# Kernel tuning notes

Hardware: AMD Instinct MI355X
Metric: run time of the kernel (lower is better)

The kernel has to match this reference:

```python
import jax, jax.numpy as jnp
import numpy as np

B, T = 256, 512
D_L, D_T, D_W, D_S = 64, 32, 32, 32
XPRIME, HIDDEN = 256, 512


def setup_inputs() -> dict:
    key = jax.random.key(0)
    ks = jax.random.split(key, 11)
    s = 0.05
    return {
        "x_l_seq": jax.random.normal(ks[0], (B, T, D_L), jnp.float32),
        "x_t_seq": jax.random.normal(ks[1], (B, T, D_T), jnp.float32),
        "x_w_seq": jax.random.normal(ks[2], (B, T, D_W), jnp.float32),
        "x_s_seq": jax.random.normal(ks[3], (B, T, D_S), jnp.float32),
        "W_ih": jax.random.normal(ks[4], (3 * HIDDEN, XPRIME), jnp.float32) * s,
        "W_hh": jax.random.normal(ks[5], (3 * HIDDEN, HIDDEN), jnp.float32) * s,
        "b_ih": jax.random.normal(ks[6], (3 * HIDDEN,), jnp.float32) * s,
        "b_hh": jax.random.normal(ks[7], (3 * HIDDEN,), jnp.float32) * s,
        "Wt_h": jax.random.normal(ks[8], (XPRIME, HIDDEN), jnp.float32) * s,
        "Wt_x": jax.random.normal(ks[9], (XPRIME, D_L + D_T + D_W + D_S), jnp.float32) * s,
        "bt": jax.random.normal(ks[10], (XPRIME,), jnp.float32) * s,
    }


def reference(x_l_seq, x_t_seq, x_w_seq, x_s_seq, W_ih, W_hh, b_ih, b_hh, Wt_h, Wt_x, bt):
    # concat the four feature streams once: [B, T, D_tot]
    x_cat = jnp.concatenate([x_l_seq, x_t_seq, x_w_seq, x_s_seq], axis=-1)
    H = W_hh.shape[1]
    Bb = x_cat.shape[0]

    def step(h, x_t):  # h: [B,H], x_t: [B,D_tot]
        # transform_block: per-step meta transform fused with recurrence
        x_prime = jnp.tanh(h @ Wt_h.T + x_t @ Wt_x.T + bt)  # [B, XPRIME]
        # torch nn.GRU cell (gate order r, z, n)
        gx = x_prime @ W_ih.T + b_ih  # [B, 3H]
        gh = h @ W_hh.T + b_hh        # [B, 3H]
        xr, xz, xn = gx[:, :H], gx[:, H:2 * H], gx[:, 2 * H:]
        hr, hz, hn = gh[:, :H], gh[:, H:2 * H], gh[:, 2 * H:]
        r = jax.nn.sigmoid(xr + hr)
        z = jax.nn.sigmoid(xz + hz)
        n = jnp.tanh(xn + r * hn)
        h_new = (1.0 - z) * n + z * h
        return h_new, None

    h0 = jnp.zeros((Bb, H), x_cat.dtype)
    hT, _ = jax.lax.scan(step, h0, jnp.swapaxes(x_cat, 0, 1))  # scan over T
    return hT[None, :, :]  # [num_layers=1, B, H]
```

## Files before the change

kernel.cpp:

```cpp
#include <hip/hip_runtime.h>
#include <math.h>

typedef __attribute__((ext_vector_type(8))) short short8;
typedef __attribute__((ext_vector_type(4))) float floatx4;
typedef __attribute__((ext_vector_type(4))) unsigned uintx4;

#define NB 256
#define NH 512
#define NXP 256
#define NT 512
#define GHP 100

#define MFMA __builtin_amdgcn_mfma_f32_16x16x32_bf16

__device__ __forceinline__ unsigned short f2bf(float f) {
    union { float f; unsigned u; } x; x.f = f;
    unsigned r = x.u + 0x7FFFu + ((x.u >> 16) & 1u);
    return (unsigned short)(r >> 16);
}
__device__ __forceinline__ float sigmoidf_(float x) { return 1.0f / (1.0f + __expf(-x)); }

__device__ __forceinline__ short8 cvt8(float4 u, float4 v) {
    short8 r;
    r[0] = (short)f2bf(u.x); r[1] = (short)f2bf(u.y);
    r[2] = (short)f2bf(u.z); r[3] = (short)f2bf(u.w);
    r[4] = (short)f2bf(v.x); r[5] = (short)f2bf(v.y);
    r[6] = (short)f2bf(v.z); r[7] = (short)f2bf(v.w);
    return r;
}

__device__ __forceinline__ void ldg4_c(const void* p0, const void* p1,
                                       const void* p2, const void* p3,
                                       uintx4& r0, uintx4& r1, uintx4& r2, uintx4& r3) {
    asm volatile(
        "global_load_dwordx4 %0, %4, off sc0 sc1\n\t"
        "global_load_dwordx4 %1, %5, off sc0 sc1\n\t"
        "global_load_dwordx4 %2, %6, off sc0 sc1\n\t"
        "global_load_dwordx4 %3, %7, off sc0 sc1\n\t"
        "s_waitcnt vmcnt(0)"
        : "=&v"(r0), "=&v"(r1), "=&v"(r2), "=&v"(r3)
        : "v"(p0), "v"(p1), "v"(p2), "v"(p3) : "memory");
}
__device__ __forceinline__ void ldg2_c(const void* p0, const void* p1,
                                       uintx4& r0, uintx4& r1) {
    asm volatile(
        "global_load_dwordx4 %0, %2, off sc0 sc1\n\t"
        "global_load_dwordx4 %1, %3, off sc0 sc1\n\t"
        "s_waitcnt vmcnt(0)"
        : "=&v"(r0), "=&v"(r1) : "v"(p0), "v"(p1) : "memory");
}
__device__ __forceinline__ void st16_c(void* p, unsigned v) {
    asm volatile("global_store_short %0, %1, off sc0 sc1" :: "v"(p), "v"(v) : "memory");
}
__device__ __forceinline__ void st32_c(void* p, unsigned v) {
    asm volatile("global_store_dword %0, %1, off sc0 sc1" :: "v"(p), "v"(v) : "memory");
}
__device__ __forceinline__ void vm_drain() {
    asm volatile("s_waitcnt vmcnt(0)" ::: "memory");
}

__device__ __forceinline__ void flag_set(int* f, int v) {
    __hip_atomic_store(f, v, __ATOMIC_RELAXED, __HIP_MEMORY_SCOPE_AGENT);
}
__device__ __forceinline__ void poll16(const int* f, int target, int lane) {
    const int* fp = f + (lane & 15) * 16;
    for (;;) {
        int v = __hip_atomic_load(fp, __ATOMIC_RELAXED, __HIP_MEMORY_SCOPE_AGENT);
        if (__ballot(v < target) == 0ull) break;
        __builtin_amdgcn_s_sleep(1);
    }
}

__global__ void k_cvt(const float* __restrict__ src, unsigned short* __restrict__ dst, int n) {
    int i = blockIdx.x * blockDim.x + threadIdx.x;
    int stride = gridDim.x * blockDim.x;
    for (; i < n; i += stride) dst[i] = f2bf(src[i]);
}

struct KParams {
    const float *xl, *xt, *xw, *xs;
    const float *bih, *bhh, *bt;
    const unsigned short *Wihb, *Whhb, *Wthb, *Wtxb;
    unsigned short *hb0, *hb1, *xpb;
    float *out;
    int *flags;
};

__global__ __launch_bounds__(256, 1)
void k_persist(KParams P)
{
    const int tid   = threadIdx.x;
    const int w     = tid >> 6;
    const int lane  = tid & 63;
    const int lr    = lane & 15;
    const int lkrow = lane >> 4;
    const int lk    = lkrow * 8;
    const int bid   = blockIdx.x;
    const int grp   = bid >> 4;
    const int jc    = bid & 15;
    const int m0    = grp * 16;
    const int j0    = jc * 32;
    const int n0    = jc * 16;

    int* gfl = P.flags + grp * 512;
    int* hfl = gfl;
    int* xfl = gfl + 256;

    __shared__ unsigned short sh_h[16 * 512];
    __shared__ unsigned short sh_xp[16 * 256];
    __shared__ float sh_gh[16 * GHP];
    __shared__ float sh_gx[2][16 * GHP];
    __shared__ float sh_b[6][32];
    __shared__ float sh_bt[16];

    if (tid < 32) {
        sh_b[0][tid] = P.bih[j0 + tid];
        sh_b[1][tid] = P.bih[512 + j0 + tid];
        sh_b[2][tid] = P.bih[1024 + j0 + tid];
        sh_b[3][tid] = P.bhh[j0 + tid];
        sh_b[4][tid] = P.bhh[512 + j0 + tid];
        sh_b[5][tid] = P.bhh[1024 + j0 + tid];
    }
    if (tid < 16) sh_bt[tid] = P.bt[n0 + tid];

    float hold0 = 0.f, hold1 = 0.f;

    short8 bWih[3][4];
    short8 bWhh[2][16];
    #pragma unroll
    for (int i = 0; i < 3; ++i) {
        const int u = w * 3 + i, tile = u >> 1, kh = u & 1;
        const int g = tile >> 1, sub = tile & 1;
        const unsigned short* bp =
            P.Wihb + (size_t)(g * 512 + j0 + sub * 16 + lr) * NXP + kh * 128 + lk;
        #pragma unroll
        for (int kb = 0; kb < 4; ++kb) bWih[i][kb] = *(const short8*)(bp + kb * 32);
    }
    if (w < 3) {
        #pragma unroll
        for (int sub = 0; sub < 2; ++sub) {
            const unsigned short* bp =
                P.Whhb + (size_t)(w * 512 + j0 + sub * 16 + lr) * NH + lk;
            #pragma unroll
            for (int kb = 0; kb < 16; ++kb) bWhh[sub][kb] = *(const short8*)(bp + kb * 32);
        }
    } else {
        const unsigned short* bp = P.Wthb + (size_t)(n0 + lr) * NH + lk;
        #pragma unroll
        for (int kb = 0; kb < 16; ++kb) bWhh[0][kb] = *(const short8*)(bp + kb * 32);
        const unsigned short* bx = P.Wtxb + (size_t)(n0 + lr) * 160 + lk;
        #pragma unroll
        for (int c = 0; c < 5; ++c) bWhh[1][c] = *(const short8*)(bx + c * 32);
    }
    __syncthreads();

    for (int t = 0; t < NT; ++t) {
        const unsigned short* hsrc = (t & 1) ? P.hb1 : P.hb0;
        unsigned short*       hdst = (t & 1) ? P.hb0 : P.hb1;

        float4 xq[5][2];
        if (w == 3) {
            const size_t r = (size_t)(m0 + lr);
            #pragma unroll
            for (int c = 0; c < 5; ++c) {
                const float* pa = (c < 2) ? P.xl + (r * NT + t) * 64 + c * 32 + lk
                                : (c == 2)? P.xt + (r * NT + t) * 32 + lk
                                : (c == 3)? P.xw + (r * NT + t) * 32 + lk
                                          : P.xs + (r * NT + t) * 32 + lk;
                xq[c][0] = *(const float4*)pa;
                xq[c][1] = *(const float4*)(pa + 4);
            }
        }

        poll16(hfl, t, lane);
        {
            const int row = tid & 15, c = (tid >> 4) * 32;
            const unsigned short* gp = hsrc + (size_t)(m0 + row) * NH + c;
            uintx4 r0, r1, r2, r3;
            ldg4_c(gp, gp + 8, gp + 16, gp + 24, r0, r1, r2, r3);
            const int sw = (row & 7) * 8;
            *(uintx4*)&sh_h[row * 512 + ((c +  0) ^ sw)] = r0;
            *(uintx4*)&sh_h[row * 512 + ((c +  8) ^ sw)] = r1;
            *(uintx4*)&sh_h[row * 512 + ((c + 16) ^ sw)] = r2;
            *(uintx4*)&sh_h[row * 512 + ((c + 24) ^ sw)] = r3;
        }
        __syncthreads();

        if (w < 3) {
            floatx4 a0 = (floatx4){0.f,0.f,0.f,0.f};
            floatx4 a1 = (floatx4){0.f,0.f,0.f,0.f};
            const int sw = (lr & 7) * 8;
            #pragma unroll
            for (int kb = 0; kb < 16; ++kb) {
                short8 a = *(const short8*)&sh_h[lr * 512 + ((kb * 32 + lk) ^ sw)];
                a0 = MFMA(a, bWhh[0][kb], a0, 0, 0, 0);
                a1 = MFMA(a, bWhh[1][kb], a1, 0, 0, 0);
            }
            #pragma unroll
            for (int rg = 0; rg < 4; ++rg) {
                const int row = lkrow * 4 + rg;
                sh_gh[row * GHP + w * 32 + lr]      = a0[rg];
                sh_gh[row * GHP + w * 32 + 16 + lr] = a1[rg];
            }
        } else {
            floatx4 acc = (floatx4){0.f,0.f,0.f,0.f};
            const int sw = (lr & 7) * 8;
            #pragma unroll
            for (int kb = 0; kb < 16; ++kb) {
                short8 a = *(const short8*)&sh_h[lr * 512 + ((kb * 32 + lk) ^ sw)];
                acc = MFMA(a, bWhh[0][kb], acc, 0, 0, 0);
            }
            #pragma unroll
            for (int c = 0; c < 5; ++c) {
                short8 a = cvt8(xq[c][0], xq[c][1]);
                acc = MFMA(a, bWhh[1][c], acc, 0, 0, 0);
            }
            #pragma unroll
            for (int rg = 0; rg < 4; ++rg) {
                const int row = lkrow * 4 + rg;
                unsigned short v = f2bf(tanhf(acc[rg] + sh_bt[lr]));
                st16_c(P.xpb + (size_t)(m0 + row) * NXP + n0 + lr, (unsigned)v);
            }
            vm_drain();
            if (lane == 0) flag_set(xfl + jc * 16, t + 1);
        }

        poll16(xfl, t + 1, lane);
        {
            const int row = tid & 15, c = (tid >> 4) * 16;
            const unsigned short* gp = P.xpb + (size_t)(m0 + row) * NXP + c;
            uintx4 r0, r1;
            ldg2_c(gp, gp + 8, r0, r1);
            const int sw = (row & 7) * 8;
            *(uintx4*)&sh_xp[row * 256 + ((c + 0) ^ sw)] = r0;
            *(uintx4*)&sh_xp[row * 256 + ((c + 8) ^ sw)] = r1;
        }
        __syncthreads();

        #pragma unroll
        for (int i = 0; i < 3; ++i) {
            const int u = w * 3 + i, tile = u >> 1, kh = u & 1;
            const int g = tile >> 1, sub = tile & 1;
            floatx4 acc = (floatx4){0.f,0.f,0.f,0.f};
            const int sw = (lr & 7) * 8;
            #pragma unroll
            for (int kb = 0; kb < 4; ++kb) {
                short8 a = *(const short8*)&sh_xp[lr * 256 + ((kh * 128 + kb * 32 + lk) ^ sw)];
                acc = MFMA(a, bWih[i][kb], acc, 0, 0, 0);
            }
            #pragma unroll
            for (int rg = 0; rg < 4; ++rg) {
                const int row = lkrow * 4 + rg;
                sh_gx[kh][row * GHP + g * 32 + sub * 16 + lr] = acc[rg];
            }
        }
        __syncthreads();

        {
            const int row = tid >> 4, jj = (tid & 15) * 2;
            float hn[2];
            #pragma unroll
            for (int jo = 0; jo < 2; ++jo) {
                const int j = jj + jo;
                float gxr = sh_gx[0][row * GHP + j]      + sh_gx[1][row * GHP + j];
                float gxz = sh_gx[0][row * GHP + 32 + j] + sh_gx[1][row * GHP + 32 + j];
                float gxn = sh_gx[0][row * GHP + 64 + j] + sh_gx[1][row * GHP + 64 + j];
                float ghr = sh_gh[row * GHP + j];
                float ghz = sh_gh[row * GHP + 32 + j];
                float ghn = sh_gh[row * GHP + 64 + j];
                float rg_ = sigmoidf_(gxr + ghr + sh_b[0][j] + sh_b[3][j]);
                float zg  = sigmoidf_(gxz + ghz + sh_b[1][j] + sh_b[4][j]);
                float ng  = tanhf(gxn + sh_b[2][j] + rg_ * (ghn + sh_b[5][j]));
                float hold = jo ? hold1 : hold0;
                hn[jo] = (1.f - zg) * ng + zg * hold;
            }
            hold0 = hn[0]; hold1 = hn[1];
            unsigned d = (unsigned)f2bf(hn[0]) | ((unsigned)f2bf(hn[1]) << 16);
            st32_c(hdst + (size_t)(m0 + row) * NH + j0 + jj, d);
            if (t == NT - 1) {
                float2 o; o.x = hn[0]; o.y = hn[1];
                *(float2*)&P.out[(size_t)(m0 + row) * NH + j0 + jj] = o;
            }
            vm_drain();
        }
        __syncthreads();
        if (tid == 0) flag_set(hfl + jc * 16, t + 1);
    }
}

extern "C" void kernel_launch(void* const* d_in, const int* in_sizes, int n_in,
                              void* d_out, int out_size, void* d_ws, size_t ws_size,
                              hipStream_t stream)
{
    (void)in_sizes; (void)n_in; (void)out_size;
    const float* xl  = (const float*)d_in[0];
    const float* xt_ = (const float*)d_in[1];
    const float* xw  = (const float*)d_in[2];
    const float* xs  = (const float*)d_in[3];
    const float* Wih = (const float*)d_in[4];
    const float* Whh = (const float*)d_in[5];
    const float* bih = (const float*)d_in[6];
    const float* bhh = (const float*)d_in[7];
    const float* Wth = (const float*)d_in[8];
    const float* Wtx = (const float*)d_in[9];
    const float* bt  = (const float*)d_in[10];

    char* p = (char*)d_ws;
    int* flags = (int*)p;                       p += 32768;
    unsigned short* hb0 = (unsigned short*)p;   p += (size_t)NB * NH * 2;
    unsigned short* hb1 = (unsigned short*)p;   p += (size_t)NB * NH * 2;
    unsigned short* xpb = (unsigned short*)p;   p += (size_t)NB * NXP * 2;
    unsigned short* Wihb = (unsigned short*)p;  p += (size_t)1536 * 256 * 2;
    unsigned short* Whhb = (unsigned short*)p;  p += (size_t)1536 * 512 * 2;
    unsigned short* Wthb = (unsigned short*)p;  p += (size_t)256 * 512 * 2;
    unsigned short* Wtxb = (unsigned short*)p;  p += (size_t)256 * 160 * 2;
    if ((size_t)(p - (char*)d_ws) > ws_size) return;

    k_cvt<<<256, 256, 0, stream>>>(Wih, Wihb, 1536 * 256);
    k_cvt<<<256, 256, 0, stream>>>(Whh, Whhb, 1536 * 512);
    k_cvt<<<64, 256, 0, stream>>>(Wth, Wthb, 256 * 512);
    k_cvt<<<32, 256, 0, stream>>>(Wtx, Wtxb, 256 * 160);
    hipMemsetAsync(flags, 0, 32768, stream);
    hipMemsetAsync(hb0, 0, (size_t)NB * NH * 2, stream);

    KParams P;
    P.xl = xl; P.xt = xt_; P.xw = xw; P.xs = xs;
    P.bih = bih; P.bhh = bhh; P.bt = bt;
    P.Wihb = Wihb; P.Whhb = Whhb; P.Wthb = Wthb; P.Wtxb = Wtxb;
    P.hb0 = hb0; P.hb1 = hb1; P.xpb = xpb;
    P.out = (float*)d_out; P.flags = flags;

    void* args[] = { &P };
    if (hipLaunchCooperativeKernel((const void*)k_persist, dim3(256), dim3(256),
                                   args, 0, stream) != hipSuccess) {
        k_persist<<<256, 256, 0, stream>>>(P);
    }
}
```

Before: 3.247 ms.

## Compute full x_prime redundantly per block to drop cross-block exchange barrier

Each block now computes the whole 16x256 x_prime tile locally (every warp does 64 columns via MFMA with Wt_h/Wt_x held in registers) instead of each block computing 16 columns, writing them to global memory, and polling a second flag set. This removes one global store/flag/poll/reload round per timestep. To free registers, W_hh fragments are now streamed from global/L2 every step instead of staying in registers. tanhf is also replaced by an exp-based approximation. The cost is 16x redundant transform-GEMM work per group and extra weight load traffic on the critical path.

```diff
diff --git a/kernel.cpp b/kernel.cpp
--- a/kernel.cpp
+++ b/kernel.cpp
@@ -19,6 +19,10 @@
     return (unsigned short)(r >> 16);
 }
 __device__ __forceinline__ float sigmoidf_(float x) { return 1.0f / (1.0f + __expf(-x)); }
+__device__ __forceinline__ float tanhf_(float x) {
+    float e = __expf(2.f * x);
+    return 1.f - 2.f / (e + 1.f);
+}
 
 __device__ __forceinline__ short8 cvt8(float4 u, float4 v) {
     short8 r;
@@ -41,17 +45,6 @@
         : "=&v"(r0), "=&v"(r1), "=&v"(r2), "=&v"(r3)
         : "v"(p0), "v"(p1), "v"(p2), "v"(p3) : "memory");
 }
-__device__ __forceinline__ void ldg2_c(const void* p0, const void* p1,
-                                       uintx4& r0, uintx4& r1) {
-    asm volatile(
-        "global_load_dwordx4 %0, %2, off sc0 sc1\n\t"
-        "global_load_dwordx4 %1, %3, off sc0 sc1\n\t"
-        "s_waitcnt vmcnt(0)"
-        : "=&v"(r0), "=&v"(r1) : "v"(p0), "v"(p1) : "memory");
-}
-__device__ __forceinline__ void st16_c(void* p, unsigned v) {
-    asm volatile("global_store_short %0, %1, off sc0 sc1" :: "v"(p), "v"(v) : "memory");
-}
 __device__ __forceinline__ void st32_c(void* p, unsigned v) {
     asm volatile("global_store_dword %0, %1, off sc0 sc1" :: "v"(p), "v"(v) : "memory");
 }
@@ -81,7 +74,7 @@
     const float *xl, *xt, *xw, *xs;
     const float *bih, *bhh, *bt;
     const unsigned short *Wihb, *Whhb, *Wthb, *Wtxb;
-    unsigned short *hb0, *hb1, *xpb;
+    unsigned short *hb0, *hb1;
     float *out;
     int *flags;
 };
@@ -100,18 +93,16 @@
     const int jc    = bid & 15;
     const int m0    = grp * 16;
     const int j0    = jc * 32;
-    const int n0    = jc * 16;
-
-    int* gfl = P.flags + grp * 512;
-    int* hfl = gfl;
-    int* xfl = gfl + 256;
+    const int xb    = w * 64;
+
+    int* hfl = P.flags + grp * 512;
 
     __shared__ unsigned short sh_h[16 * 512];
     __shared__ unsigned short sh_xp[16 * 256];
     __shared__ float sh_gh[16 * GHP];
     __shared__ float sh_gx[2][16 * GHP];
     __shared__ float sh_b[6][32];
-    __shared__ float sh_bt[16];
+    __shared__ float sh_bt[256];
 
     if (tid < 32) {
         sh_b[0][tid] = P.bih[j0 + tid];
@@ -121,12 +112,22 @@
         sh_b[4][tid] = P.bhh[512 + j0 + tid];
         sh_b[5][tid] = P.bhh[1024 + j0 + tid];
     }
-    if (tid < 16) sh_bt[tid] = P.bt[n0 + tid];
+    sh_bt[tid] = P.bt[tid];
 
     float hold0 = 0.f, hold1 = 0.f;
 
+    short8 bWt[4][16];
+    short8 bWtx[4][5];
     short8 bWih[3][4];
-    short8 bWhh[2][16];
+    #pragma unroll
+    for (int tl = 0; tl < 4; ++tl) {
+        const unsigned short* bp = P.Wthb + (size_t)(xb + tl * 16 + lr) * NH + lk;
+        #pragma unroll
+        for (int kb = 0; kb < 16; ++kb) bWt[tl][kb] = *(const short8*)(bp + kb * 32);
+        const unsigned short* bx = P.Wtxb + (size_t)(xb + tl * 16 + lr) * 160 + lk;
+        #pragma unroll
+        for (int c = 0; c < 5; ++c) bWtx[tl][c] = *(const short8*)(bx + c * 32);
+    }
     #pragma unroll
     for (int i = 0; i < 3; ++i) {
         const int u = w * 3 + i, tile = u >> 1, kh = u & 1;
@@ -136,39 +137,54 @@
         #pragma unroll
         for (int kb = 0; kb < 4; ++kb) bWih[i][kb] = *(const short8*)(bp + kb * 32);
     }
-    if (w < 3) {
-        #pragma unroll
-        for (int sub = 0; sub < 2; ++sub) {
-            const unsigned short* bp =
-                P.Whhb + (size_t)(w * 512 + j0 + sub * 16 + lr) * NH + lk;
-            #pragma unroll
-            for (int kb = 0; kb < 16; ++kb) bWhh[sub][kb] = *(const short8*)(bp + kb * 32);
-        }
-    } else {
-        const unsigned short* bp = P.Wthb + (size_t)(n0 + lr) * NH + lk;
-        #pragma unroll
-        for (int kb = 0; kb < 16; ++kb) bWhh[0][kb] = *(const short8*)(bp + kb * 32);
-        const unsigned short* bx = P.Wtxb + (size_t)(n0 + lr) * 160 + lk;
-        #pragma unroll
-        for (int c = 0; c < 5; ++c) bWhh[1][c] = *(const short8*)(bx + c * 32);
-    }
+    const unsigned short* whh0 = P.Whhb + (size_t)(w * 512 + j0 + lr) * NH + lk;
+    const unsigned short* whh1 = P.Whhb + (size_t)(w * 512 + j0 + 16 + lr) * NH + lk;
     __syncthreads();
 
     for (int t = 0; t < NT; ++t) {
         const unsigned short* hsrc = (t & 1) ? P.hb1 : P.hb0;
         unsigned short*       hdst = (t & 1) ? P.hb0 : P.hb1;
 
-        float4 xq[5][2];
-        if (w == 3) {
+        floatx4 axp[4];
+        axp[0] = (floatx4){0.f,0.f,0.f,0.f}; axp[1] = (floatx4){0.f,0.f,0.f,0.f};
+        axp[2] = (floatx4){0.f,0.f,0.f,0.f}; axp[3] = (floatx4){0.f,0.f,0.f,0.f};
+        {
             const size_t r = (size_t)(m0 + lr);
-            #pragma unroll
-            for (int c = 0; c < 5; ++c) {
-                const float* pa = (c < 2) ? P.xl + (r * NT + t) * 64 + c * 32 + lk
-                                : (c == 2)? P.xt + (r * NT + t) * 32 + lk
-                                : (c == 3)? P.xw + (r * NT + t) * 32 + lk
-                                          : P.xs + (r * NT + t) * 32 + lk;
-                xq[c][0] = *(const float4*)pa;
-                xq[c][1] = *(const float4*)(pa + 4);
+            {
+                float4 q[3][2];
+                #pragma unroll
+                for (int c = 0; c < 3; ++c) {
+                    const float* pa = (c < 2) ? P.xl + (r * NT + t) * 64 + c * 32 + lk
+                                              : P.xt + (r * NT + t) * 32 + lk;
+                    q[c][0] = *(const float4*)pa;
+                    q[c][1] = *(const float4*)(pa + 4);
+                }
+                #pragma unroll
+                for (int c = 0; c < 3; ++c) {
+                    short8 a = cvt8(q[c][0], q[c][1]);
+                    axp[0] = MFMA(a, bWtx[0][c], axp[0], 0, 0, 0);
+                    axp[1] = MFMA(a, bWtx[1][c], axp[1], 0, 0, 0);
+                    axp[2] = MFMA(a, bWtx[2][c], axp[2], 0, 0, 0);
+                    axp[3] = MFMA(a, bWtx[3][c], axp[3], 0, 0, 0);
+                }
+            }
+            {
+                float4 q[2][2];
+                #pragma unroll
+                for (int c = 0; c < 2; ++c) {
+                    const float* pa = (c == 0) ? P.xw + (r * NT + t) * 32 + lk
+                                               : P.xs + (r * NT + t) * 32 + lk;
+                    q[c][0] = *(const float4*)pa;
+                    q[c][1] = *(const float4*)(pa + 4);
+                }
+                #pragma unroll
+                for (int c = 0; c < 2; ++c) {
+                    short8 a = cvt8(q[c][0], q[c][1]);
+                    axp[0] = MFMA(a, bWtx[0][c + 3], axp[0], 0, 0, 0);
+                    axp[1] = MFMA(a, bWtx[1][c + 3], axp[1], 0, 0, 0);
+                    axp[2] = MFMA(a, bWtx[2][c + 3], axp[2], 0, 0, 0);
+                    axp[3] = MFMA(a, bWtx[3][c + 3], axp[3], 0, 0, 0);
+                }
             }
         }
 
@@ -186,15 +202,39 @@
         }
         __syncthreads();
 
+        {
+            const int sw = (lr & 7) * 8;
+            #pragma unroll
+            for (int kb = 0; kb < 16; ++kb) {
+                short8 a = *(const short8*)&sh_h[lr * 512 + ((kb * 32 + lk) ^ sw)];
+                axp[0] = MFMA(a, bWt[0][kb], axp[0], 0, 0, 0);
+                axp[1] = MFMA(a, bWt[1][kb], axp[1], 0, 0, 0);
+                axp[2] = MFMA(a, bWt[2][kb], axp[2], 0, 0, 0);
+                axp[3] = MFMA(a, bWt[3][kb], axp[3], 0, 0, 0);
+            }
+        }
+        #pragma unroll
+        for (int tl = 0; tl < 4; ++tl) {
+            #pragma unroll
+            for (int rg = 0; rg < 4; ++rg) {
+                const int m = lkrow * 4 + rg;
+                const int n = xb + tl * 16 + lr;
+                sh_xp[m * 256 + (n ^ ((m & 7) * 8))] =
+                    f2bf(tanhf_(axp[tl][rg] + sh_bt[n]));
+            }
+        }
+
         if (w < 3) {
             floatx4 a0 = (floatx4){0.f,0.f,0.f,0.f};
             floatx4 a1 = (floatx4){0.f,0.f,0.f,0.f};
             const int sw = (lr & 7) * 8;
             #pragma unroll
             for (int kb = 0; kb < 16; ++kb) {
-                short8 a = *(const short8*)&sh_h[lr * 512 + ((kb * 32 + lk) ^ sw)];
-                a0 = MFMA(a, bWhh[0][kb], a0, 0, 0, 0);
-                a1 = MFMA(a, bWhh[1][kb], a1, 0, 0, 0);
+                short8 a  = *(const short8*)&sh_h[lr * 512 + ((kb * 32 + lk) ^ sw)];
+                short8 b0 = *(const short8*)(whh0 + kb * 32);
+                short8 b1 = *(const short8*)(whh1 + kb * 32);
+                a0 = MFMA(a, b0, a0, 0, 0, 0);
+                a1 = MFMA(a, b1, a1, 0, 0, 0);
             }
             #pragma unroll
             for (int rg = 0; rg < 4; ++rg) {
@@ -202,38 +242,6 @@
                 sh_gh[row * GHP + w * 32 + lr]      = a0[rg];
                 sh_gh[row * GHP + w * 32 + 16 + lr] = a1[rg];
             }
-        } else {
-            floatx4 acc = (floatx4){0.f,0.f,0.f,0.f};
-            const int sw = (lr & 7) * 8;
-            #pragma unroll
-            for (int kb = 0; kb < 16; ++kb) {
-                short8 a = *(const short8*)&sh_h[lr * 512 + ((kb * 32 + lk) ^ sw)];
-                acc = MFMA(a, bWhh[0][kb], acc, 0, 0, 0);
-            }
-            #pragma unroll
-            for (int c = 0; c < 5; ++c) {
-                short8 a = cvt8(xq[c][0], xq[c][1]);
-                acc = MFMA(a, bWhh[1][c], acc, 0, 0, 0);
-            }
-            #pragma unroll
-            for (int rg = 0; rg < 4; ++rg) {
-                const int row = lkrow * 4 + rg;
-                unsigned short v = f2bf(tanhf(acc[rg] + sh_bt[lr]));
-                st16_c(P.xpb + (size_t)(m0 + row) * NXP + n0 + lr, (unsigned)v);
-            }
-            vm_drain();
-            if (lane == 0) flag_set(xfl + jc * 16, t + 1);
-        }
-
-        poll16(xfl, t + 1, lane);
-        {
-            const int row = tid & 15, c = (tid >> 4) * 16;
-            const unsigned short* gp = P.xpb + (size_t)(m0 + row) * NXP + c;
-            uintx4 r0, r1;
-            ldg2_c(gp, gp + 8, r0, r1);
-            const int sw = (row & 7) * 8;
-            *(uintx4*)&sh_xp[row * 256 + ((c + 0) ^ sw)] = r0;
-            *(uintx4*)&sh_xp[row * 256 + ((c + 8) ^ sw)] = r1;
         }
         __syncthreads();
 
@@ -270,7 +278,7 @@
                 float ghn = sh_gh[row * GHP + 64 + j];
                 float rg_ = sigmoidf_(gxr + ghr + sh_b[0][j] + sh_b[3][j]);
                 float zg  = sigmoidf_(gxz + ghz + sh_b[1][j] + sh_b[4][j]);
-                float ng  = tanhf(gxn + sh_b[2][j] + rg_ * (ghn + sh_b[5][j]));
+                float ng  = tanhf_(gxn + sh_b[2][j] + rg_ * (ghn + sh_b[5][j]));
                 float hold = jo ? hold1 : hold0;
                 hn[jo] = (1.f - zg) * ng + zg * hold;
             }
@@ -309,7 +317,6 @@
     int* flags = (int*)p;                       p += 32768;
     unsigned short* hb0 = (unsigned short*)p;   p += (size_t)NB * NH * 2;
     unsigned short* hb1 = (unsigned short*)p;   p += (size_t)NB * NH * 2;
-    unsigned short* xpb = (unsigned short*)p;   p += (size_t)NB * NXP * 2;
     unsigned short* Wihb = (unsigned short*)p;  p += (size_t)1536 * 256 * 2;
     unsigned short* Whhb = (unsigned short*)p;  p += (size_t)1536 * 512 * 2;
     unsigned short* Wthb = (unsigned short*)p;  p += (size_t)256 * 512 * 2;
@@ -327,7 +334,7 @@
     P.xl = xl; P.xt = xt_; P.xw = xw; P.xs = xs;
     P.bih = bih; P.bhh = bhh; P.bt = bt;
     P.Wihb = Wihb; P.Whhb = Whhb; P.Wthb = Wthb; P.Wtxb = Wtxb;
-    P.hb0 = hb0; P.hb1 = hb1; P.xpb = xpb;
+    P.hb0 = hb0; P.hb1 = hb1;
     P.out = (float*)d_out; P.flags = flags;
 
     void* args[] = { &P };
```

Result: slower. 4.896 ms (+50.8%).

## Replace x' flag handshake with step-tagged data words polled directly

Applied to the files above, without the earlier changes.

Each x' element is now stored as a 32-bit word carrying the bf16 value in the low half and the step number in the high half. Consumers poll the data itself until every tag matches the current step, which removes the producer's store drain, the flag store and the separate flag poll from the per-step critical path. In exchange it doubles the x' buffer traffic, adds an extra memset, and relies on each 32-bit store being seen atomically. Consumers may also reissue loads many times while spinning.

```diff
diff --git a/kernel.cpp b/kernel.cpp
--- a/kernel.cpp
+++ b/kernel.cpp
@@ -41,16 +41,9 @@
         : "=&v"(r0), "=&v"(r1), "=&v"(r2), "=&v"(r3)
         : "v"(p0), "v"(p1), "v"(p2), "v"(p3) : "memory");
 }
-__device__ __forceinline__ void ldg2_c(const void* p0, const void* p1,
-                                       uintx4& r0, uintx4& r1) {
-    asm volatile(
-        "global_load_dwordx4 %0, %2, off sc0 sc1\n\t"
-        "global_load_dwordx4 %1, %3, off sc0 sc1\n\t"
-        "s_waitcnt vmcnt(0)"
-        : "=&v"(r0), "=&v"(r1) : "v"(p0), "v"(p1) : "memory");
-}
-__device__ __forceinline__ void st16_c(void* p, unsigned v) {
-    asm volatile("global_store_short %0, %1, off sc0 sc1" :: "v"(p), "v"(v) : "memory");
+__device__ __forceinline__ void ldg4_nw(const void* p, uintx4& r) {
+    asm volatile("global_load_dwordx4 %0, %1, off sc0 sc1"
+                 : "=&v"(r) : "v"(p) : "memory");
 }
 __device__ __forceinline__ void st32_c(void* p, unsigned v) {
     asm volatile("global_store_dword %0, %1, off sc0 sc1" :: "v"(p), "v"(v) : "memory");
@@ -81,7 +74,8 @@
     const float *xl, *xt, *xw, *xs;
     const float *bih, *bhh, *bt;
     const unsigned short *Wihb, *Whhb, *Wthb, *Wtxb;
-    unsigned short *hb0, *hb1, *xpb;
+    unsigned short *hb0, *hb1;
+    unsigned *xT;
     float *out;
     int *flags;
 };
@@ -102,9 +96,7 @@
     const int j0    = jc * 32;
     const int n0    = jc * 16;
 
-    int* gfl = P.flags + grp * 512;
-    int* hfl = gfl;
-    int* xfl = gfl + 256;
+    int* hfl = P.flags + grp * 512;
 
     __shared__ unsigned short sh_h[16 * 512];
     __shared__ unsigned short sh_xp[16 * 256];
@@ -215,25 +207,47 @@
                 short8 a = cvt8(xq[c][0], xq[c][1]);
                 acc = MFMA(a, bWhh[1][c], acc, 0, 0, 0);
             }
+            const unsigned xtag = ((unsigned)(t + 1)) << 16;
             #pragma unroll
             for (int rg = 0; rg < 4; ++rg) {
                 const int row = lkrow * 4 + rg;
                 unsigned short v = f2bf(tanhf(acc[rg] + sh_bt[lr]));
-                st16_c(P.xpb + (size_t)(m0 + row) * NXP + n0 + lr, (unsigned)v);
-            }
-            vm_drain();
-            if (lane == 0) flag_set(xfl + jc * 16, t + 1);
-        }
-
-        poll16(xfl, t + 1, lane);
+                st32_c(P.xT + (size_t)(m0 + row) * NXP + n0 + lr, xtag | (unsigned)v);
+            }
+        }
+
         {
             const int row = tid & 15, c = (tid >> 4) * 16;
-            const unsigned short* gp = P.xpb + (size_t)(m0 + row) * NXP + c;
-            uintx4 r0, r1;
-            ldg2_c(gp, gp + 8, r0, r1);
+            const unsigned* bp = P.xT + (size_t)(m0 + row) * NXP + c;
+            uintx4 B[4];
+            unsigned pend = 0xFu;
+            const unsigned tg = (unsigned)(t + 1);
+            for (;;) {
+                #pragma unroll
+                for (int b = 0; b < 4; ++b)
+                    if (pend & (1u << b)) ldg4_nw(bp + b * 4, B[b]);
+                vm_drain();
+                __builtin_amdgcn_sched_barrier(0);
+                #pragma unroll
+                for (int b = 0; b < 4; ++b)
+                    if (pend & (1u << b)) {
+                        if ((B[b][0] >> 16) == tg && (B[b][1] >> 16) == tg &&
+                            (B[b][2] >> 16) == tg && (B[b][3] >> 16) == tg)
+                            pend &= ~(1u << b);
+                    }
+                if (__ballot(pend != 0u) == 0ull) break;
+                __builtin_amdgcn_s_sleep(1);
+            }
             const int sw = (row & 7) * 8;
-            *(uintx4*)&sh_xp[row * 256 + ((c + 0) ^ sw)] = r0;
-            *(uintx4*)&sh_xp[row * 256 + ((c + 8) ^ sw)] = r1;
+            #pragma unroll
+            for (int q = 0; q < 2; ++q) {
+                uintx4 pk;
+                pk[0] = (B[2*q][0]   & 0xffffu) | (B[2*q][1]   << 16);
+                pk[1] = (B[2*q][2]   & 0xffffu) | (B[2*q][3]   << 16);
+                pk[2] = (B[2*q+1][0] & 0xffffu) | (B[2*q+1][1] << 16);
+                pk[3] = (B[2*q+1][2] & 0xffffu) | (B[2*q+1][3] << 16);
+                *(uintx4*)&sh_xp[row * 256 + ((c + 8 * q) ^ sw)] = pk;
+            }
         }
         __syncthreads();
 
@@ -307,9 +321,9 @@
 
     char* p = (char*)d_ws;
     int* flags = (int*)p;                       p += 32768;
+    unsigned* xT = (unsigned*)p;                p += (size_t)NB * NXP * 4;
     unsigned short* hb0 = (unsigned short*)p;   p += (size_t)NB * NH * 2;
     unsigned short* hb1 = (unsigned short*)p;   p += (size_t)NB * NH * 2;
-    unsigned short* xpb = (unsigned short*)p;   p += (size_t)NB * NXP * 2;
     unsigned short* Wihb = (unsigned short*)p;  p += (size_t)1536 * 256 * 2;
     unsigned short* Whhb = (unsigned short*)p;  p += (size_t)1536 * 512 * 2;
     unsigned short* Wthb = (unsigned short*)p;  p += (size_t)256 * 512 * 2;
@@ -321,13 +335,14 @@
     k_cvt<<<64, 256, 0, stream>>>(Wth, Wthb, 256 * 512);
     k_cvt<<<32, 256, 0, stream>>>(Wtx, Wtxb, 256 * 160);
     hipMemsetAsync(flags, 0, 32768, stream);
+    hipMemsetAsync(xT, 0, (size_t)NB * NXP * 4, stream);
     hipMemsetAsync(hb0, 0, (size_t)NB * NH * 2, stream);
 
     KParams P;
     P.xl = xl; P.xt = xt_; P.xw = xw; P.xs = xs;
     P.bih = bih; P.bhh = bhh; P.bt = bt;
     P.Wihb = Wihb; P.Whhb = Whhb; P.Wthb = Wthb; P.Wtxb = Wtxb;
-    P.hb0 = hb0; P.hb1 = hb1; P.xpb = xpb;
+    P.hb0 = hb0; P.hb1 = hb1; P.xT = xT;
     P.out = (float*)d_out; P.flags = flags;
 
     void* args[] = { &P };
```

Result: slower. 4.041 ms (median of 2 runs) (+24.5%).
